# Kernel optimization log

Hardware: AMD Instinct MI355X
Metric: run time of the kernel (lower is better)

Reference implementation:

```python
import jax, jax.numpy as jnp
import numpy as np

H, W = 85, 85
N_HEAD = 8

def layernorm(x, g, b, eps=1e-5):
    m = x.mean(-1, keepdims=True)
    v = ((x - m) ** 2).mean(-1, keepdims=True)
    return (x - m) * jax.lax.rsqrt(v + eps) * g + b


def setup_inputs() -> dict:
    key = jax.random.key(0)
    ks = jax.random.split(key, 12)
    B, C = 8, 256
    N = H * W
    hd = C // N_HEAD
    Ch = C * 4  # mlp_ratio = 4
    init = lambda k, fan_in, sh: (jax.random.normal(k, sh, jnp.float32) / np.float32(np.sqrt(fan_in)))
    d = {}
    d['fx'] = jax.random.normal(ks[0], (B, N, C), jnp.float32)
    # ln_1
    d['ln1_g'] = jnp.ones((C,), jnp.float32); d['ln1_b'] = jnp.zeros((C,), jnp.float32)
    # Galerkin linear attention projections (per-head split of C)
    d['Wq'] = init(ks[1], C, (C, C)); d['bq'] = jnp.zeros((C,), jnp.float32)
    d['Wk'] = init(ks[2], C, (C, C)); d['bk'] = jnp.zeros((C,), jnp.float32)
    d['Wv'] = init(ks[3], C, (C, C)); d['bv'] = jnp.zeros((C,), jnp.float32)
    d['Wo'] = init(ks[4], C, (C, C)); d['bo'] = jnp.zeros((C,), jnp.float32)
    # per-head LayerNorms on K and V (Galerkin normalization replacing softmax)
    d['kln_g'] = jnp.ones((N_HEAD, hd), jnp.float32); d['kln_b'] = jnp.zeros((N_HEAD, hd), jnp.float32)
    d['vln_g'] = jnp.ones((N_HEAD, hd), jnp.float32); d['vln_b'] = jnp.zeros((N_HEAD, hd), jnp.float32)
    # ln_2
    d['ln2_g'] = jnp.ones((C,), jnp.float32); d['ln2_b'] = jnp.zeros((C,), jnp.float32)
    # MLP (n_layers=0, res=False): pre linear + gelu, post linear
    d['W1'] = init(ks[5], C, (C, Ch)); d['b1'] = jnp.zeros((Ch,), jnp.float32)
    d['W2'] = init(ks[6], Ch, (Ch, C)); d['b2'] = jnp.zeros((C,), jnp.float32)
    return d


def reference(fx, ln1_g, ln1_b, Wq, bq, Wk, bk, Wv, bv, Wo, bo,
              kln_g, kln_b, vln_g, vln_b, ln2_g, ln2_b, W1, b1, W2, b2):
    B, N, C = fx.shape
    hd = C // N_HEAD
    x = layernorm(fx, ln1_g, ln1_b)  # [B,N,C]
    # (permute/reshape to image grid and back is a no-op for per-token attention math)
    split = lambda t: t.reshape(B, N, N_HEAD, hd).transpose(0, 2, 1, 3)  # [B,h,N,d]
    q = split(x @ Wq + bq)
    k = split(x @ Wk + bk)
    v = split(x @ Wv + bv)
    # Galerkin: LayerNorm on K and V over head dim, no softmax
    k = layernorm(k, kln_g[None, :, None, :], kln_b[None, :, None, :])
    v = layernorm(v, vln_g[None, :, None, :], vln_b[None, :, None, :])
    kv = jnp.einsum('bhnd,bhne->bhde', k, v) / N  # [B,h,d,d]
    attn = jnp.einsum('bhnd,bhde->bhne', q, kv)   # [B,h,N,d]
    attn = attn.transpose(0, 2, 1, 3).reshape(B, N, C)
    attn = attn @ Wo + bo
    fx = fx + attn  # residual 1
    x2 = layernorm(fx, ln2_g, ln2_b)
    x2 = jax.nn.gelu(x2 @ W1 + b1) @ W2 + b2
    return fx + x2  # residual 2
```

## Files before the change

### kernel.cpp

```cpp
#include <hip/hip_runtime.h>
#include <hip/hip_bf16.h>
#include <stdint.h>

#define B_ 8
#define NTOK 7225
#define MTOT (B_*NTOK)
#define MROWS 58368
#define RT_FULL 452
#define RT_BATCH 57

typedef unsigned short u16;
typedef u16 u16x8 __attribute__((ext_vector_type(8)));
typedef u16 u16x4 __attribute__((ext_vector_type(4)));
typedef __bf16 bf16x8 __attribute__((ext_vector_type(8)));
typedef float f32x4 __attribute__((ext_vector_type(4)));

__device__ inline float bf2f(u16 u){ union{float f;uint32_t i;}c; c.i=((uint32_t)u)<<16; return c.f; }
__device__ inline u16 f2bf(float f){ union{float f;uint32_t i;}c; c.f=f; uint32_t x=c.i;
                                     return (u16)((x + 0x7fffu + ((x>>16)&1u))>>16); }
__device__ inline uint32_t cvt_pk_bf16(float a, float b){
  uint32_t r; asm("v_cvt_pk_bf16_f32 %0, %1, %2" : "=v"(r) : "v"(a), "v"(b)); return r;
}
__device__ inline float gelu_f(float x){
  float t = 0.7978845608028654f * x * (1.0f + 0.044715f*x*x);
  float e = __expf(2.0f*t);
  return x * (1.0f - __builtin_amdgcn_rcpf(e + 1.0f));
}

__device__ inline void gload_lds16(const u16* g, u16* l) {
  __builtin_amdgcn_global_load_lds(
      (__attribute__((address_space(1))) void*)(const_cast<u16*>(g)),
      (__attribute__((address_space(3))) void*)(l), 16, 0, 0);
}

template<int EPI>
__global__ __launch_bounds__(256)
void gemm_bt(const u16* __restrict__ A, int lda,
             const u16* __restrict__ B, int ldb, int bStride,
             const float* __restrict__ bias,
             const float* __restrict__ res,
             void* __restrict__ outp, int ldo,
             int K, int rowsValid, int batchRowStride)
{
  __shared__ alignas(16) u16 As[2][128][32];
  __shared__ alignas(16) u16 Bs[2][128][32];
  const int tid = threadIdx.x;
  const int wid = tid >> 6;
  const int lane = tid & 63;

  const int gx = gridDim.x, gy = gridDim.y;
  const int n = gx * gy;
  const int flat = blockIdx.y * gx + blockIdx.x;
  const int qq = n >> 3, rr = n & 7;
  const int xcd = flat & 7, pos = flat >> 3;
  const int swz = (xcd < rr ? xcd*(qq+1) : rr*(qq+1) + (xcd-rr)*qq) + pos;
  const int bx = swz / gy, by = swz % gy;

  const int bz = blockIdx.z;
  const long rowBase = (long)bz * batchRowStride + (long)bx * 128;
  const int colBase = by * 128;
  const u16* Bp = B + (long)bz * bStride;

  const int srow = lane >> 2;
  const int scol = ((lane & 3) ^ ((lane >> 3) & 3)) * 8;
  const int NTk = K >> 5;

  auto stage = [&](int bf, int kt) {
    const int k0 = kt << 5;
#pragma unroll
    for (int i = 0; i < 2; ++i) {
      int r = wid*32 + i*16 + srow;
      gload_lds16(A + (rowBase + r)*(long)lda + k0 + scol, &As[bf][wid*32 + i*16][0]);
    }
#pragma unroll
    for (int i = 0; i < 2; ++i) {
      int r = wid*32 + i*16 + srow;
      gload_lds16(Bp + (long)(colBase + r)*ldb + k0 + scol, &Bs[bf][wid*32 + i*16][0]);
    }
  };

  f32x4 acc[4][4] = {};
  const int wm = wid >> 1, wn = wid & 1;
  const int lr = lane & 15;
  const int sl = lane >> 4;

  stage(0, 0);
  for (int kt = 0; kt < NTk; ++kt) {
    const int bf = kt & 1;
    __syncthreads();
    if (kt + 1 < NTk) stage(bf ^ 1, kt + 1);
    bf16x8 a[4], b[4];
#pragma unroll
    for (int mi = 0; mi < 4; ++mi) {
      const int r = wm*64 + mi*16 + lr;
      const int sp = sl ^ ((r >> 1) & 3);
      a[mi] = *reinterpret_cast<const bf16x8*>(&As[bf][r][sp*8]);
    }
#pragma unroll
    for (int ni = 0; ni < 4; ++ni) {
      const int r = wn*64 + ni*16 + lr;
      const int sp = sl ^ ((r >> 1) & 3);
      b[ni] = *reinterpret_cast<const bf16x8*>(&Bs[bf][r][sp*8]);
    }
#pragma unroll
    for (int mi = 0; mi < 4; ++mi)
#pragma unroll
      for (int ni = 0; ni < 4; ++ni)
        acc[mi][ni] = __builtin_amdgcn_mfma_f32_16x16x32_bf16(b[ni], a[mi], acc[mi][ni], 0, 0, 0);
  }

  const int cq = (lane >> 4) * 4;
  f32x4 bv4[4];
#pragma unroll
  for (int ni = 0; ni < 4; ++ni)
    bv4[ni] = *reinterpret_cast<const f32x4*>(&bias[colBase + wn*64 + ni*16 + cq]);
#pragma unroll
  for (int mi = 0; mi < 4; ++mi) {
    const int r = wm*64 + mi*16 + lr;
    if (bx*128 + r < rowsValid) {
      const long grow = rowBase + r;
#pragma unroll
      for (int ni = 0; ni < 4; ++ni) {
        const int c0 = colBase + wn*64 + ni*16 + cq;
        const long oidx = grow*(long)ldo + c0;
        f32x4 v = acc[mi][ni] + bv4[ni];
        if (EPI == 0) {
          uint2 pk; pk.x = cvt_pk_bf16(v[0], v[1]); pk.y = cvt_pk_bf16(v[2], v[3]);
          *reinterpret_cast<uint2*>((u16*)outp + oidx) = pk;
        } else if (EPI == 1) {
          uint2 pk; pk.x = cvt_pk_bf16(gelu_f(v[0]), gelu_f(v[1]));
          pk.y = cvt_pk_bf16(gelu_f(v[2]), gelu_f(v[3]));
          *reinterpret_cast<uint2*>((u16*)outp + oidx) = pk;
        } else {
          f32x4 rv = *reinterpret_cast<const f32x4*>((const float*)res + oidx);
          *reinterpret_cast<f32x4*>((float*)outp + oidx) = v + rv;
        }
      }
    }
  }
}

__global__ __launch_bounds__(256)
void ln_kernel(const float* __restrict__ in, const float* __restrict__ g,
               const float* __restrict__ bt, u16* __restrict__ out, int M)
{
  const int wv = threadIdx.x >> 6, lane = threadIdx.x & 63;
  const int t = blockIdx.x * 4 + wv;
  if (t >= M) return;
  const float4 x = reinterpret_cast<const float4*>(in + (long)t*256)[lane];
  float s = x.x + x.y + x.z + x.w;
  float q = x.x*x.x + x.y*x.y + x.z*x.z + x.w*x.w;
#pragma unroll
  for (int o = 32; o > 0; o >>= 1) { s += __shfl_xor(s, o); q += __shfl_xor(q, o); }
  const float m  = s * (1.0f/256.0f);
  const float var = q * (1.0f/256.0f) - m*m;
  const float rs = rsqrtf(var + 1e-5f);
  const float4 gv = reinterpret_cast<const float4*>(g)[lane];
  const float4 bv = reinterpret_cast<const float4*>(bt)[lane];
  uint2 o4;
  o4.x = cvt_pk_bf16((x.x - m)*rs*gv.x + bv.x, (x.y - m)*rs*gv.y + bv.y);
  o4.y = cvt_pk_bf16((x.z - m)*rs*gv.z + bv.z, (x.w - m)*rs*gv.w + bv.w);
  *reinterpret_cast<uint2*>(out + (long)t*256 + lane*4) = o4;
}

__global__ __launch_bounds__(256)
void kv_kernel(const u16* __restrict__ QKV,
               const float* __restrict__ kg, const float* __restrict__ kb,
               const float* __restrict__ vg, const float* __restrict__ vb,
               float* __restrict__ kvout)
{
  const int bh = blockIdx.x, b = bh >> 3, h = bh & 7;
  const int tid = threadIdx.x;
  __shared__ u16 kls[256][32];
  __shared__ u16 vls[256][32];
  __shared__ float sg[4][32];
  if (tid < 32) {
    sg[0][tid] = kg[h*32 + tid];
    sg[1][tid] = kb[h*32 + tid];
    sg[2][tid] = vg[h*32 + tid];
    sg[3][tid] = vb[h*32 + tid];
  }
  const int d = tid >> 3, e0 = (tid & 7) * 4;
  float a0=0, a1=0, a2=0, a3=0;

  for (int sub = 0; sub < 2; ++sub) {
    const int r = blockIdx.y * 512 + sub * 256 + tid;
    __syncthreads();
    if (r < NTOK) {
      const u16* rowp = QKV + (long)(b*NTOK + r)*768;
#pragma unroll
      for (int kv2 = 0; kv2 < 2; ++kv2) {
        const u16* p = rowp + (kv2 ? 512 : 256) + h*32;
        float xv[32]; float s = 0.f;
#pragma unroll
        for (int q4 = 0; q4 < 4; ++q4) {
          u16x8 u = *reinterpret_cast<const u16x8*>(p + q4*8);
#pragma unroll
          for (int j = 0; j < 8; ++j) { float f = bf2f(u[j]); xv[q4*8+j] = f; s += f; }
        }
        const float m = s * (1.0f/32.0f);
        float vv = 0.f;
#pragma unroll
        for (int j = 0; j < 32; ++j) { float d2 = xv[j]-m; vv += d2*d2; }
        const float rs = rsqrtf(vv*(1.0f/32.0f) + 1e-5f);
        const float* gg = sg[kv2 ? 2 : 0];
        const float* bb = sg[kv2 ? 3 : 1];
        u16 (*dst)[32] = kv2 ? vls : kls;
#pragma unroll
        for (int j = 0; j < 32; ++j) dst[tid][j] = f2bf((xv[j]-m)*rs*gg[j] + bb[j]);
      }
    } else {
#pragma unroll
      for (int j = 0; j < 32; ++j) { kls[tid][j] = 0; vls[tid][j] = 0; }
    }
    __syncthreads();
#pragma unroll 4
    for (int rr = 0; rr < 256; ++rr) {
      const float kd = bf2f(kls[rr][d]);
      u16x4 v4 = *reinterpret_cast<const u16x4*>(&vls[rr][e0]);
      a0 += kd * bf2f(v4[0]); a1 += kd * bf2f(v4[1]);
      a2 += kd * bf2f(v4[2]); a3 += kd * bf2f(v4[3]);
    }
  }
  const float sc = 1.0f / (float)NTOK;
  float* o = kvout + (long)bh*1024 + d*32 + e0;
  atomicAdd(o+0, a0*sc); atomicAdd(o+1, a1*sc);
  atomicAdd(o+2, a2*sc); atomicAdd(o+3, a3*sc);
}

__global__ __launch_bounds__(256)
void woeff_kernel(const float* __restrict__ kv, const float* __restrict__ Wo,
                  u16* __restrict__ Woet)
{
  const int b = blockIdx.x >> 8, c = blockIdx.x & 255;
  const int rtid = threadIdx.x;
  const int h = rtid >> 5, dd = rtid & 31;
  const float* kvp = kv + ((long)(b*8 + h)*32 + dd)*32;
  float s = 0.f;
#pragma unroll 8
  for (int e = 0; e < 32; ++e) s += kvp[e] * Wo[(h*32 + e)*256 + c];
  Woet[(long)(b*256 + c)*256 + rtid] = f2bf(s);
}

__global__ void zero_f32(float* p, int n) {
  int i = blockIdx.x*blockDim.x + threadIdx.x; if (i < n) p[i] = 0.f;
}
__global__ void concat_bias(const float* bq, const float* bk, const float* bv, float* o) {
  int i = threadIdx.x;
  o[i] = (i < 256) ? bq[i] : ((i < 512) ? bk[i-256] : bv[i-512]);
}
__global__ __launch_bounds__(256)
void transpose_cvt(const float* __restrict__ src, u16* __restrict__ dst, int R, int C) {
  __shared__ float t[32][33];
  const int tc = blockIdx.x * 32, tr = blockIdx.y * 32;
  const int lx = threadIdx.x & 31, ly = threadIdx.x >> 5;
#pragma unroll
  for (int i = 0; i < 32; i += 8)
    t[ly + i][lx] = src[(long)(tr + ly + i)*C + tc + lx];
  __syncthreads();
#pragma unroll
  for (int i = 0; i < 32; i += 8)
    dst[(long)(tc + ly + i)*R + tr + lx] = f2bf(t[lx][ly + i]);
}

extern "C" void kernel_launch(void* const* d_in, const int* in_sizes, int n_in,
                              void* d_out, int out_size, void* d_ws, size_t ws_size,
                              hipStream_t stream)
{
  const float* fx    = (const float*)d_in[0];
  const float* ln1_g = (const float*)d_in[1];
  const float* ln1_b = (const float*)d_in[2];
  const float* Wq = (const float*)d_in[3];
  const float* bq = (const float*)d_in[4];
  const float* Wk = (const float*)d_in[5];
  const float* bk = (const float*)d_in[6];
  const float* Wv = (const float*)d_in[7];
  const float* bv = (const float*)d_in[8];
  const float* Wo = (const float*)d_in[9];
  const float* bo = (const float*)d_in[10];
  const float* kg  = (const float*)d_in[11];
  const float* kbb = (const float*)d_in[12];
  const float* vg  = (const float*)d_in[13];
  const float* vbb = (const float*)d_in[14];
  const float* ln2_g = (const float*)d_in[15];
  const float* ln2_b = (const float*)d_in[16];
  const float* W1 = (const float*)d_in[17];
  const float* b1 = (const float*)d_in[18];
  const float* W2 = (const float*)d_in[19];
  const float* b2 = (const float*)d_in[20];
  float* outF = (float*)d_out;

  char* ws = (char*)d_ws;
  size_t off = 0;
  auto alloc = [&](size_t bytes) { char* p = ws + off; off += (bytes + 255) & ~(size_t)255; return p; };
  u16* bufX   = (u16*)alloc((size_t)MROWS*256*2);
  u16* bufQKV = (u16*)alloc((size_t)MROWS*768*2);
  u16* bufH   = (u16*)alloc((size_t)MROWS*1024*2);
  u16* Wqkv_t = (u16*)alloc(768*256*2);
  u16* W1_t   = (u16*)alloc(1024*256*2);
  u16* W2_t   = (u16*)alloc(256*1024*2);
  u16* Woe_t  = (u16*)alloc((size_t)8*256*256*2);
  float* kvb  = (float*)alloc((size_t)64*1024*4);
  float* bqkv = (float*)alloc(768*4);
  (void)ws_size; (void)out_size; (void)n_in; (void)in_sizes;

  zero_f32<<<256, 256, 0, stream>>>(kvb, 65536);
  concat_bias<<<1, 768, 0, stream>>>(bq, bk, bv, bqkv);
  transpose_cvt<<<dim3(8,8),  256, 0, stream>>>(Wq, Wqkv_t,          256, 256);
  transpose_cvt<<<dim3(8,8),  256, 0, stream>>>(Wk, Wqkv_t + 65536,  256, 256);
  transpose_cvt<<<dim3(8,8),  256, 0, stream>>>(Wv, Wqkv_t + 131072, 256, 256);
  transpose_cvt<<<dim3(32,8), 256, 0, stream>>>(W1, W1_t, 256, 1024);
  transpose_cvt<<<dim3(8,32), 256, 0, stream>>>(W2, W2_t, 1024, 256);

  ln_kernel<<<MTOT/4, 256, 0, stream>>>(fx, ln1_g, ln1_b, bufX, MTOT);

  gemm_bt<0><<<dim3(RT_FULL, 6, 1), 256, 0, stream>>>(
      bufX, 256, Wqkv_t, 256, 0, bqkv, nullptr, bufQKV, 768, 256, 1<<30, 0);

  kv_kernel<<<dim3(64, 15), 256, 0, stream>>>(bufQKV, kg, kbb, vg, vbb, kvb);

  woeff_kernel<<<2048, 256, 0, stream>>>(kvb, Wo, Woe_t);

  gemm_bt<2><<<dim3(RT_BATCH, 2, 8), 256, 0, stream>>>(
      bufQKV, 768, Woe_t, 256, 65536, bo, fx, outF, 256, 256, NTOK, NTOK);

  ln_kernel<<<MTOT/4, 256, 0, stream>>>(outF, ln2_g, ln2_b, bufX, MTOT);

  gemm_bt<1><<<dim3(RT_FULL, 8, 1), 256, 0, stream>>>(
      bufX, 256, W1_t, 256, 0, b1, nullptr, bufH, 1024, 256, 1<<30, 0);

  gemm_bt<2><<<dim3(RT_FULL, 2, 1), 256, 0, stream>>>(
      bufH, 1024, W2_t, 1024, 0, b2, outF, outF, 256, 1024, MTOT, 0);
}
```

Measured before the change: 331.4 us.

## Deepen GEMM LDS pipeline to four buffers with explicit vmcnt waits

The bf16 GEMM's LDS staging goes from double buffering to a four-slot ring that keeps three K-tiles of global-to-LDS loads in flight. The per-iteration __syncthreads is replaced by explicit s_waitcnt vmcnt counts, a raw barrier and a sched_barrier, with the last two tiles handled in a peeled epilogue. The aim is to hide global memory latency behind MFMA work. In exchange, shared memory per block doubles to 64 KB, which can lower occupancy, and correctness now depends on the hand-counted vmcnt values matching the four loads each stage issues.

```diff
diff --git a/kernel.cpp b/kernel.cpp
--- a/kernel.cpp
+++ b/kernel.cpp
@@ -42,8 +42,8 @@
              void* __restrict__ outp, int ldo,
              int K, int rowsValid, int batchRowStride)
 {
-  __shared__ alignas(16) u16 As[2][128][32];
-  __shared__ alignas(16) u16 Bs[2][128][32];
+  __shared__ alignas(16) u16 As[4][128][32];
+  __shared__ alignas(16) u16 Bs[4][128][32];
   const int tid = threadIdx.x;
   const int wid = tid >> 6;
   const int lane = tid & 63;
@@ -65,17 +65,17 @@
   const int scol = ((lane & 3) ^ ((lane >> 3) & 3)) * 8;
   const int NTk = K >> 5;
 
-  auto stage = [&](int bf, int kt) {
+  auto stage = [&](int bi, int kt) {
     const int k0 = kt << 5;
 #pragma unroll
     for (int i = 0; i < 2; ++i) {
       int r = wid*32 + i*16 + srow;
-      gload_lds16(A + (rowBase + r)*(long)lda + k0 + scol, &As[bf][wid*32 + i*16][0]);
+      gload_lds16(A + (rowBase + r)*(long)lda + k0 + scol, &As[bi][wid*32 + i*16][0]);
     }
 #pragma unroll
     for (int i = 0; i < 2; ++i) {
       int r = wid*32 + i*16 + srow;
-      gload_lds16(Bp + (long)(colBase + r)*ldb + k0 + scol, &Bs[bf][wid*32 + i*16][0]);
+      gload_lds16(Bp + (long)(colBase + r)*ldb + k0 + scol, &Bs[bi][wid*32 + i*16][0]);
     }
   };
 
@@ -84,30 +84,44 @@
   const int lr = lane & 15;
   const int sl = lane >> 4;
 
-  stage(0, 0);
-  for (int kt = 0; kt < NTk; ++kt) {
-    const int bf = kt & 1;
-    __syncthreads();
-    if (kt + 1 < NTk) stage(bf ^ 1, kt + 1);
+  auto compute = [&](int bi) {
     bf16x8 a[4], b[4];
 #pragma unroll
     for (int mi = 0; mi < 4; ++mi) {
       const int r = wm*64 + mi*16 + lr;
       const int sp = sl ^ ((r >> 1) & 3);
-      a[mi] = *reinterpret_cast<const bf16x8*>(&As[bf][r][sp*8]);
+      a[mi] = *reinterpret_cast<const bf16x8*>(&As[bi][r][sp*8]);
     }
 #pragma unroll
     for (int ni = 0; ni < 4; ++ni) {
       const int r = wn*64 + ni*16 + lr;
       const int sp = sl ^ ((r >> 1) & 3);
-      b[ni] = *reinterpret_cast<const bf16x8*>(&Bs[bf][r][sp*8]);
+      b[ni] = *reinterpret_cast<const bf16x8*>(&Bs[bi][r][sp*8]);
     }
 #pragma unroll
     for (int mi = 0; mi < 4; ++mi)
 #pragma unroll
       for (int ni = 0; ni < 4; ++ni)
         acc[mi][ni] = __builtin_amdgcn_mfma_f32_16x16x32_bf16(b[ni], a[mi], acc[mi][ni], 0, 0, 0);
+  };
+
+  stage(0, 0); stage(1, 1); stage(2, 2);
+
+  for (int kt = 0; kt < NTk - 2; ++kt) {
+    asm volatile("s_waitcnt vmcnt(8)" ::: "memory");
+    __builtin_amdgcn_s_barrier();
+    __builtin_amdgcn_sched_barrier(0);
+    if (kt < NTk - 3) stage((kt + 3) & 3, kt + 3);
+    compute(kt & 3);
   }
+  asm volatile("s_waitcnt vmcnt(4)" ::: "memory");
+  __builtin_amdgcn_s_barrier();
+  __builtin_amdgcn_sched_barrier(0);
+  compute((NTk - 2) & 3);
+  asm volatile("s_waitcnt vmcnt(0)" ::: "memory");
+  __builtin_amdgcn_s_barrier();
+  __builtin_amdgcn_sched_barrier(0);
+  compute((NTk - 1) & 3);
 
   const int cq = (lane >> 4) * 4;
   f32x4 bv4[4];
```

New measurement: 340.9 us. 1.03x slower.

## Replace tiled GEMMs with persistent streaming GEMM using 128-wide K chunks

Applied to the files above, without the earlier changes.

Swaps the per-tile 256-thread GEMM grid for a persistent kernel of 256 blocks × 512 threads. Each block walks a contiguous range of output tiles as one continuous stream of 128-wide K chunks, double-buffered in 128 KB of LDS with direct global-to-LDS loads and explicit vmcnt waits. The aim is to overlap the loads for the next tile with the math and epilogue of the current one, and to cut launch and tail overhead. In exchange, LDS use rises sharply, occupancy drops to one block per CU, and each wave holds fewer accumulators (32×64), so it has to hide latency mainly through prefetch depth.

```diff
diff --git a/kernel.cpp b/kernel.cpp
--- a/kernel.cpp
+++ b/kernel.cpp
@@ -6,8 +6,6 @@
 #define NTOK 7225
 #define MTOT (B_*NTOK)
 #define MROWS 58368
-#define RT_FULL 452
-#define RT_BATCH 57
 
 typedef unsigned short u16;
 typedef u16 u16x8 __attribute__((ext_vector_type(8)));
@@ -33,107 +31,133 @@
       (__attribute__((address_space(3))) void*)(l), 16, 0, 0);
 }
 
-template<int EPI>
-__global__ __launch_bounds__(256)
-void gemm_bt(const u16* __restrict__ A, int lda,
-             const u16* __restrict__ B, int ldb, int bStride,
-             const float* __restrict__ bias,
-             const float* __restrict__ res,
-             void* __restrict__ outp, int ldo,
-             int K, int rowsValid, int batchRowStride)
-{
-  __shared__ alignas(16) u16 As[2][128][32];
-  __shared__ alignas(16) u16 Bs[2][128][32];
+template<int EPI, int NC>
+__global__ __launch_bounds__(512)
+void gemm_stream(const u16* __restrict__ A, int lda,
+                 const u16* __restrict__ Bm, int ldb, long bStride,
+                 const float* __restrict__ bias,
+                 const float* __restrict__ res,
+                 void* __restrict__ outp, int ldo,
+                 int ntM, int ntN, int nTiles,
+                 int rowsValid, int batchRowStride)
+{
+  __shared__ alignas(16) u16 lds[2][32768];
   const int tid = threadIdx.x;
-  const int wid = tid >> 6;
-  const int lane = tid & 63;
-
-  const int gx = gridDim.x, gy = gridDim.y;
-  const int n = gx * gy;
-  const int flat = blockIdx.y * gx + blockIdx.x;
-  const int qq = n >> 3, rr = n & 7;
-  const int xcd = flat & 7, pos = flat >> 3;
-  const int swz = (xcd < rr ? xcd*(qq+1) : rr*(qq+1) + (xcd-rr)*qq) + pos;
-  const int bx = swz / gy, by = swz % gy;
-
-  const int bz = blockIdx.z;
-  const long rowBase = (long)bz * batchRowStride + (long)bx * 128;
-  const int colBase = by * 128;
-  const u16* Bp = B + (long)bz * bStride;
-
-  const int srow = lane >> 2;
-  const int scol = ((lane & 3) ^ ((lane >> 3) & 3)) * 8;
-  const int NTk = K >> 5;
-
-  auto stage = [&](int bf, int kt) {
-    const int k0 = kt << 5;
-#pragma unroll
-    for (int i = 0; i < 2; ++i) {
-      int r = wid*32 + i*16 + srow;
-      gload_lds16(A + (rowBase + r)*(long)lda + k0 + scol, &As[bf][wid*32 + i*16][0]);
-    }
-#pragma unroll
-    for (int i = 0; i < 2; ++i) {
-      int r = wid*32 + i*16 + srow;
-      gload_lds16(Bp + (long)(colBase + r)*ldb + k0 + scol, &Bs[bf][wid*32 + i*16][0]);
+  const int wid = tid >> 6, lane = tid & 63;
+  const int wm = wid >> 1, wn = wid & 1;
+  const int lr = lane & 15, sl = lane >> 4;
+
+  const int nb = gridDim.x;
+  const int q = nTiles / nb, rem = nTiles % nb;
+  const int p = blockIdx.x;
+  const int t0 = p * q + (p < rem ? p : rem);
+  const int myT = q + (p < rem ? 1 : 0);
+  const int U = myT * NC;
+
+  auto stage = [&](int u, int bi) {
+    const int t = t0 + u / NC, ch = u % NC;
+    int rel = t; const int bz = rel / (ntM*ntN); rel -= bz*(ntM*ntN);
+    const int bx = rel / ntN, by = rel - bx*ntN;
+    const long rowB = (long)bz * batchRowStride + (long)bx * 128;
+    const long colB = (long)by * 128;
+    const u16* Bp = Bm + (long)bz * bStride;
+    const int k0 = ch << 7;
+#pragma unroll
+    for (int i = 0; i < 4; ++i) {
+      const int o16 = i*512 + tid;
+      const int r = o16 >> 4, ps = o16 & 15;
+      const int gc = ((ps ^ (r & 7)) << 3) + k0;
+      gload_lds16(A + (rowB + r)*(long)lda + gc, &lds[bi][o16*8]);
+    }
+#pragma unroll
+    for (int i = 0; i < 4; ++i) {
+      const int o16 = i*512 + tid;
+      const int r = o16 >> 4, ps = o16 & 15;
+      const int gc = ((ps ^ (r & 7)) << 3) + k0;
+      gload_lds16(Bp + (colB + r)*(long)ldb + gc, &lds[bi][16384 + o16*8]);
     }
   };
 
-  f32x4 acc[4][4] = {};
-  const int wm = wid >> 1, wn = wid & 1;
-  const int lr = lane & 15;
-  const int sl = lane >> 4;
-
+  f32x4 acc[2][4];
   stage(0, 0);
-  for (int kt = 0; kt < NTk; ++kt) {
-    const int bf = kt & 1;
-    __syncthreads();
-    if (kt + 1 < NTk) stage(bf ^ 1, kt + 1);
-    bf16x8 a[4], b[4];
-#pragma unroll
-    for (int mi = 0; mi < 4; ++mi) {
-      const int r = wm*64 + mi*16 + lr;
-      const int sp = sl ^ ((r >> 1) & 3);
-      a[mi] = *reinterpret_cast<const bf16x8*>(&As[bf][r][sp*8]);
+  stage(1, 1);
+
+  for (int u = 0; u < U; ++u) {
+    const int bi = u & 1;
+    const int ch = u % NC;
+    if (u == U - 1) { asm volatile("s_waitcnt vmcnt(0)" ::: "memory"); }
+    else            { asm volatile("s_waitcnt vmcnt(8)" ::: "memory"); }
+    __builtin_amdgcn_s_barrier();
+
+    if (ch == 0) {
+#pragma unroll
+      for (int mi = 0; mi < 2; ++mi)
+#pragma unroll
+        for (int ni = 0; ni < 4; ++ni) acc[mi][ni] = f32x4{0.f,0.f,0.f,0.f};
+    }
+
+    bf16x8 fa[2][4], fb[4][4];
+#pragma unroll
+    for (int mi = 0; mi < 2; ++mi) {
+      const int ra = wm*32 + mi*16 + lr;
+#pragma unroll
+      for (int ks = 0; ks < 4; ++ks) {
+        const int ps = (ks*4 + sl) ^ (ra & 7);
+        fa[mi][ks] = *reinterpret_cast<const bf16x8*>(&lds[bi][ra*128 + ps*8]);
+      }
     }
 #pragma unroll
     for (int ni = 0; ni < 4; ++ni) {
-      const int r = wn*64 + ni*16 + lr;
-      const int sp = sl ^ ((r >> 1) & 3);
-      b[ni] = *reinterpret_cast<const bf16x8*>(&Bs[bf][r][sp*8]);
-    }
-#pragma unroll
-    for (int mi = 0; mi < 4; ++mi)
-#pragma unroll
-      for (int ni = 0; ni < 4; ++ni)
-        acc[mi][ni] = __builtin_amdgcn_mfma_f32_16x16x32_bf16(b[ni], a[mi], acc[mi][ni], 0, 0, 0);
-  }
-
-  const int cq = (lane >> 4) * 4;
-  f32x4 bv4[4];
-#pragma unroll
-  for (int ni = 0; ni < 4; ++ni)
-    bv4[ni] = *reinterpret_cast<const f32x4*>(&bias[colBase + wn*64 + ni*16 + cq]);
-#pragma unroll
-  for (int mi = 0; mi < 4; ++mi) {
-    const int r = wm*64 + mi*16 + lr;
-    if (bx*128 + r < rowsValid) {
-      const long grow = rowBase + r;
-#pragma unroll
-      for (int ni = 0; ni < 4; ++ni) {
-        const int c0 = colBase + wn*64 + ni*16 + cq;
-        const long oidx = grow*(long)ldo + c0;
-        f32x4 v = acc[mi][ni] + bv4[ni];
-        if (EPI == 0) {
-          uint2 pk; pk.x = cvt_pk_bf16(v[0], v[1]); pk.y = cvt_pk_bf16(v[2], v[3]);
-          *reinterpret_cast<uint2*>((u16*)outp + oidx) = pk;
-        } else if (EPI == 1) {
-          uint2 pk; pk.x = cvt_pk_bf16(gelu_f(v[0]), gelu_f(v[1]));
-          pk.y = cvt_pk_bf16(gelu_f(v[2]), gelu_f(v[3]));
-          *reinterpret_cast<uint2*>((u16*)outp + oidx) = pk;
-        } else {
-          f32x4 rv = *reinterpret_cast<const f32x4*>((const float*)res + oidx);
-          *reinterpret_cast<f32x4*>((float*)outp + oidx) = v + rv;
+      const int rb = wn*64 + ni*16 + lr;
+#pragma unroll
+      for (int ks = 0; ks < 4; ++ks) {
+        const int ps = (ks*4 + sl) ^ (rb & 7);
+        fb[ni][ks] = *reinterpret_cast<const bf16x8*>(&lds[bi][16384 + rb*128 + ps*8]);
+      }
+    }
+    asm volatile("s_waitcnt lgkmcnt(0)" ::: "memory");
+    __builtin_amdgcn_sched_barrier(0);
+    __builtin_amdgcn_s_barrier();
+
+    if (u + 2 < U) stage(u + 2, bi);
+
+#pragma unroll
+    for (int ks = 0; ks < 4; ++ks)
+#pragma unroll
+      for (int mi = 0; mi < 2; ++mi)
+#pragma unroll
+        for (int ni = 0; ni < 4; ++ni)
+          acc[mi][ni] = __builtin_amdgcn_mfma_f32_16x16x32_bf16(fb[ni][ks], fa[mi][ks], acc[mi][ni], 0, 0, 0);
+
+    if (ch == NC - 1) {
+      const int t = t0 + u / NC;
+      int rel = t; const int bz = rel / (ntM*ntN); rel -= bz*(ntM*ntN);
+      const int bx = rel / ntN, by = rel - bx*ntN;
+      const long rowB = (long)bz * batchRowStride + (long)bx * 128;
+      const int colB = by * 128;
+      const int cq = sl * 4;
+#pragma unroll
+      for (int mi = 0; mi < 2; ++mi) {
+        const int r = wm*32 + mi*16 + lr;
+        if (bx*128 + r < rowsValid) {
+          const long grow = rowB + r;
+#pragma unroll
+          for (int ni = 0; ni < 4; ++ni) {
+            const int c0 = colB + wn*64 + ni*16 + cq;
+            const long oidx = grow*(long)ldo + c0;
+            f32x4 v = acc[mi][ni] + *reinterpret_cast<const f32x4*>(&bias[c0]);
+            if (EPI == 0) {
+              uint2 pk; pk.x = cvt_pk_bf16(v[0], v[1]); pk.y = cvt_pk_bf16(v[2], v[3]);
+              *reinterpret_cast<uint2*>((u16*)outp + oidx) = pk;
+            } else if (EPI == 1) {
+              uint2 pk; pk.x = cvt_pk_bf16(gelu_f(v[0]), gelu_f(v[1]));
+              pk.y = cvt_pk_bf16(gelu_f(v[2]), gelu_f(v[3]));
+              *reinterpret_cast<uint2*>((u16*)outp + oidx) = pk;
+            } else {
+              f32x4 rv = *reinterpret_cast<const f32x4*>((const float*)res + oidx);
+              *reinterpret_cast<f32x4*>((float*)outp + oidx) = v + rv;
+            }
+          }
         }
       }
     }
@@ -314,21 +338,25 @@
 
   ln_kernel<<<MTOT/4, 256, 0, stream>>>(fx, ln1_g, ln1_b, bufX, MTOT);
 
-  gemm_bt<0><<<dim3(RT_FULL, 6, 1), 256, 0, stream>>>(
-      bufX, 256, Wqkv_t, 256, 0, bqkv, nullptr, bufQKV, 768, 256, 1<<30, 0);
+  gemm_stream<0,2><<<256, 512, 0, stream>>>(
+      bufX, 256, Wqkv_t, 256, 0, bqkv, nullptr, bufQKV, 768,
+      452, 6, 452*6, MTOT, 0);
 
   kv_kernel<<<dim3(64, 15), 256, 0, stream>>>(bufQKV, kg, kbb, vg, vbb, kvb);
 
   woeff_kernel<<<2048, 256, 0, stream>>>(kvb, Wo, Woe_t);
 
-  gemm_bt<2><<<dim3(RT_BATCH, 2, 8), 256, 0, stream>>>(
-      bufQKV, 768, Woe_t, 256, 65536, bo, fx, outF, 256, 256, NTOK, NTOK);
+  gemm_stream<2,2><<<256, 512, 0, stream>>>(
+      bufQKV, 768, Woe_t, 256, 65536, bo, fx, outF, 256,
+      57, 2, 8*57*2, NTOK, NTOK);
 
   ln_kernel<<<MTOT/4, 256, 0, stream>>>(outF, ln2_g, ln2_b, bufX, MTOT);
 
-  gemm_bt<1><<<dim3(RT_FULL, 8, 1), 256, 0, stream>>>(
-      bufX, 256, W1_t, 256, 0, b1, nullptr, bufH, 1024, 256, 1<<30, 0);
-
-  gemm_bt<2><<<dim3(RT_FULL, 2, 1), 256, 0, stream>>>(
-      bufH, 1024, W2_t, 1024, 0, b2, outF, outF, 256, 1024, MTOT, 0);
-}
+  gemm_stream<1,2><<<256, 512, 0, stream>>>(
+      bufX, 256, W1_t, 256, 0, b1, nullptr, bufH, 1024,
+      452, 8, 452*8, MTOT, 0);
+
+  gemm_stream<2,8><<<256, 512, 0, stream>>>(
+      bufH, 1024, W2_t, 1024, 0, b2, outF, outF, 256,
+      452, 2, 452*2, MTOT, 0);
+}
```

New measurement: 391.1 us. 1.18x slower.

## Fold Q projection into per-batch attention weight and enlarge GEMM tiles

Applied to the files above, without the earlier changes.

Removes the Q projection GEMM by precomputing, per batch, a combined matrix Watt = Wq·(kv·Wo) and a bias be = bq·(kv·Wo) + bo. The attention output GEMM then reads the LN1 output directly instead of stored Q, and the QKV GEMM shrinks to a KV-only GEMM. Separately, the GEMM kernel moves to 256x256 tiles with 512 threads and a K-step of 64 to raise data reuse per block. The larger tiles use more registers and shared memory and leave fewer blocks in flight, and the combined weight is rounded to bf16, which adds rounding error.

```diff
diff --git a/kernel.cpp b/kernel.cpp
--- a/kernel.cpp
+++ b/kernel.cpp
@@ -6,8 +6,8 @@
 #define NTOK 7225
 #define MTOT (B_*NTOK)
 #define MROWS 58368
-#define RT_FULL 452
-#define RT_BATCH 57
+#define MT_FULL 226
+#define MT_BATCH 29
 
 typedef unsigned short u16;
 typedef u16 u16x8 __attribute__((ext_vector_type(8)));
@@ -34,19 +34,19 @@
 }
 
 template<int EPI>
-__global__ __launch_bounds__(256)
-void gemm_bt(const u16* __restrict__ A, int lda,
-             const u16* __restrict__ B, int ldb, int bStride,
-             const float* __restrict__ bias,
+__global__ __launch_bounds__(512, 2)
+void gemm256(const u16* __restrict__ A, int lda,
+             const u16* __restrict__ Bm, int ldb, long bStride,
+             const float* __restrict__ bias, int biasStride,
              const float* __restrict__ res,
              void* __restrict__ outp, int ldo,
              int K, int rowsValid, int batchRowStride)
 {
-  __shared__ alignas(16) u16 As[2][128][32];
-  __shared__ alignas(16) u16 Bs[2][128][32];
+  __shared__ alignas(16) u16 As[2][2][256][32];
+  __shared__ alignas(16) u16 Bs[2][2][256][32];
   const int tid = threadIdx.x;
-  const int wid = tid >> 6;
-  const int lane = tid & 63;
+  const int wid = tid >> 6, lane = tid & 63;
+  const int wm = wid >> 2, wn = wid & 3;
 
   const int gx = gridDim.x, gy = gridDim.y;
   const int n = gx * gy;
@@ -55,75 +55,76 @@
   const int xcd = flat & 7, pos = flat >> 3;
   const int swz = (xcd < rr ? xcd*(qq+1) : rr*(qq+1) + (xcd-rr)*qq) + pos;
   const int bx = swz / gy, by = swz % gy;
-
   const int bz = blockIdx.z;
-  const long rowBase = (long)bz * batchRowStride + (long)bx * 128;
-  const int colBase = by * 128;
-  const u16* Bp = B + (long)bz * bStride;
+
+  const long rowBase = (long)bz * batchRowStride + (long)bx * 256;
+  const int colBase = by * 256;
+  const u16* Bp = Bm + (long)bz * bStride;
+  const float* biasP = bias + bz * biasStride;
 
   const int srow = lane >> 2;
   const int scol = ((lane & 3) ^ ((lane >> 3) & 3)) * 8;
-  const int NTk = K >> 5;
+  const int NT = K >> 6;
 
   auto stage = [&](int bf, int kt) {
-    const int k0 = kt << 5;
-#pragma unroll
-    for (int i = 0; i < 2; ++i) {
-      int r = wid*32 + i*16 + srow;
-      gload_lds16(A + (rowBase + r)*(long)lda + k0 + scol, &As[bf][wid*32 + i*16][0]);
-    }
-#pragma unroll
-    for (int i = 0; i < 2; ++i) {
-      int r = wid*32 + i*16 + srow;
-      gload_lds16(Bp + (long)(colBase + r)*ldb + k0 + scol, &Bs[bf][wid*32 + i*16][0]);
+    const int k0 = kt << 6;
+#pragma unroll
+    for (int i = 0; i < 4; ++i) {
+      const int u = wid*4 + i;
+      const int sub = u >> 4, r0 = (u & 15) * 16;
+      const int r = r0 + srow;
+      gload_lds16(A + (rowBase + r)*(long)lda + k0 + sub*32 + scol, &As[bf][sub][r0][0]);
+    }
+#pragma unroll
+    for (int i = 0; i < 4; ++i) {
+      const int u = wid*4 + i;
+      const int sub = u >> 4, r0 = (u & 15) * 16;
+      const int r = r0 + srow;
+      gload_lds16(Bp + (long)(colBase + r)*ldb + k0 + sub*32 + scol, &Bs[bf][sub][r0][0]);
     }
   };
 
-  f32x4 acc[4][4] = {};
-  const int wm = wid >> 1, wn = wid & 1;
+  f32x4 acc[8][4] = {};
   const int lr = lane & 15;
   const int sl = lane >> 4;
+  const int sp = (sl ^ ((lr >> 1) & 3)) * 8;
+
+  auto compute = [&](int bf) {
+#pragma unroll
+    for (int sub = 0; sub < 2; ++sub) {
+      bf16x8 a[8], b[4];
+#pragma unroll
+      for (int mi = 0; mi < 8; ++mi)
+        a[mi] = *reinterpret_cast<const bf16x8*>(&As[bf][sub][wm*128 + mi*16 + lr][sp]);
+#pragma unroll
+      for (int ni = 0; ni < 4; ++ni)
+        b[ni] = *reinterpret_cast<const bf16x8*>(&Bs[bf][sub][wn*64 + ni*16 + lr][sp]);
+#pragma unroll
+      for (int mi = 0; mi < 8; ++mi)
+#pragma unroll
+        for (int ni = 0; ni < 4; ++ni)
+          acc[mi][ni] = __builtin_amdgcn_mfma_f32_16x16x32_bf16(b[ni], a[mi], acc[mi][ni], 0, 0, 0);
+    }
+  };
 
   stage(0, 0);
-  for (int kt = 0; kt < NTk; ++kt) {
-    const int bf = kt & 1;
+  for (int kt = 0; kt < NT; ++kt) {
     __syncthreads();
-    if (kt + 1 < NTk) stage(bf ^ 1, kt + 1);
-    bf16x8 a[4], b[4];
-#pragma unroll
-    for (int mi = 0; mi < 4; ++mi) {
-      const int r = wm*64 + mi*16 + lr;
-      const int sp = sl ^ ((r >> 1) & 3);
-      a[mi] = *reinterpret_cast<const bf16x8*>(&As[bf][r][sp*8]);
-    }
-#pragma unroll
-    for (int ni = 0; ni < 4; ++ni) {
-      const int r = wn*64 + ni*16 + lr;
-      const int sp = sl ^ ((r >> 1) & 3);
-      b[ni] = *reinterpret_cast<const bf16x8*>(&Bs[bf][r][sp*8]);
-    }
-#pragma unroll
-    for (int mi = 0; mi < 4; ++mi)
-#pragma unroll
-      for (int ni = 0; ni < 4; ++ni)
-        acc[mi][ni] = __builtin_amdgcn_mfma_f32_16x16x32_bf16(b[ni], a[mi], acc[mi][ni], 0, 0, 0);
-  }
-
-  const int cq = (lane >> 4) * 4;
-  f32x4 bv4[4];
-#pragma unroll
-  for (int ni = 0; ni < 4; ++ni)
-    bv4[ni] = *reinterpret_cast<const f32x4*>(&bias[colBase + wn*64 + ni*16 + cq]);
-#pragma unroll
-  for (int mi = 0; mi < 4; ++mi) {
-    const int r = wm*64 + mi*16 + lr;
-    if (bx*128 + r < rowsValid) {
+    if (kt + 1 < NT) stage((kt + 1) & 1, kt + 1);
+    compute(kt & 1);
+  }
+
+  const int cq = sl * 4;
+#pragma unroll
+  for (int mi = 0; mi < 8; ++mi) {
+    const int r = wm*128 + mi*16 + lr;
+    if (bx*256 + r < rowsValid) {
       const long grow = rowBase + r;
 #pragma unroll
       for (int ni = 0; ni < 4; ++ni) {
         const int c0 = colBase + wn*64 + ni*16 + cq;
         const long oidx = grow*(long)ldo + c0;
-        f32x4 v = acc[mi][ni] + bv4[ni];
+        f32x4 v = acc[mi][ni] + *reinterpret_cast<const f32x4*>(&biasP[c0]);
         if (EPI == 0) {
           uint2 pk; pk.x = cvt_pk_bf16(v[0], v[1]); pk.y = cvt_pk_bf16(v[2], v[3]);
           *reinterpret_cast<uint2*>((u16*)outp + oidx) = pk;
@@ -164,7 +165,7 @@
 }
 
 __global__ __launch_bounds__(256)
-void kv_kernel(const u16* __restrict__ QKV,
+void kv_kernel(const u16* __restrict__ KV,
                const float* __restrict__ kg, const float* __restrict__ kb,
                const float* __restrict__ vg, const float* __restrict__ vb,
                float* __restrict__ kvout)
@@ -187,10 +188,10 @@
     const int r = blockIdx.y * 512 + sub * 256 + tid;
     __syncthreads();
     if (r < NTOK) {
-      const u16* rowp = QKV + (long)(b*NTOK + r)*768;
+      const u16* rowp = KV + (long)(b*NTOK + r)*512;
 #pragma unroll
       for (int kv2 = 0; kv2 < 2; ++kv2) {
-        const u16* p = rowp + (kv2 ? 512 : 256) + h*32;
+        const u16* p = rowp + (kv2 ? 256 : 0) + h*32;
         float xv[32]; float s = 0.f;
 #pragma unroll
         for (int q4 = 0; q4 < 4; ++q4) {
@@ -242,12 +243,50 @@
   Woet[(long)(b*256 + c)*256 + rtid] = f2bf(s);
 }
 
+__global__ __launch_bounds__(256)
+void watt_kernel(const u16* __restrict__ wq_bf, const u16* __restrict__ Woet,
+                 u16* __restrict__ Watt)
+{
+  const int b = blockIdx.x >> 8, c = blockIdx.x & 255;
+  const int k = threadIdx.x;
+  const u16* wr = wq_bf + (long)k*256;
+  const u16* er = Woet + ((long)(b*256 + c))*256;
+  float s = 0.f;
+#pragma unroll 4
+  for (int j0 = 0; j0 < 256; j0 += 8) {
+    u16x8 wv = *reinterpret_cast<const u16x8*>(wr + j0);
+    u16x8 ev = *reinterpret_cast<const u16x8*>(er + j0);
+#pragma unroll
+    for (int j = 0; j < 8; ++j) s += bf2f(wv[j]) * bf2f(ev[j]);
+  }
+  Watt[((long)(b*256 + c))*256 + k] = f2bf(s);
+}
+
+__global__ __launch_bounds__(256)
+void be_kernel(const float* __restrict__ bq, const float* __restrict__ bo,
+               const u16* __restrict__ Woet, float* __restrict__ be)
+{
+  const int b = blockIdx.x, c = threadIdx.x;
+  const u16* er = Woet + ((long)(b*256 + c))*256;
+  float s = bo[c];
+#pragma unroll 4
+  for (int j0 = 0; j0 < 256; j0 += 8) {
+    u16x8 ev = *reinterpret_cast<const u16x8*>(er + j0);
+#pragma unroll
+    for (int j = 0; j < 8; ++j) s += bq[j0+j] * bf2f(ev[j]);
+  }
+  be[b*256 + c] = s;
+}
+
 __global__ void zero_f32(float* p, int n) {
   int i = blockIdx.x*blockDim.x + threadIdx.x; if (i < n) p[i] = 0.f;
 }
-__global__ void concat_bias(const float* bq, const float* bk, const float* bv, float* o) {
+__global__ void concat_bias2(const float* bk, const float* bv, float* o) {
   int i = threadIdx.x;
-  o[i] = (i < 256) ? bq[i] : ((i < 512) ? bk[i-256] : bv[i-512]);
+  o[i] = (i < 256) ? bk[i] : bv[i-256];
+}
+__global__ void cvt_bf(const float* __restrict__ src, u16* __restrict__ dst, int n) {
+  int i = blockIdx.x*blockDim.x + threadIdx.x; if (i < n) dst[i] = f2bf(src[i]);
 }
 __global__ __launch_bounds__(256)
 void transpose_cvt(const float* __restrict__ src, u16* __restrict__ dst, int R, int C) {
@@ -294,41 +333,46 @@
   size_t off = 0;
   auto alloc = [&](size_t bytes) { char* p = ws + off; off += (bytes + 255) & ~(size_t)255; return p; };
   u16* bufX   = (u16*)alloc((size_t)MROWS*256*2);
-  u16* bufQKV = (u16*)alloc((size_t)MROWS*768*2);
+  u16* bufKV  = (u16*)alloc((size_t)MROWS*512*2);
   u16* bufH   = (u16*)alloc((size_t)MROWS*1024*2);
-  u16* Wqkv_t = (u16*)alloc(768*256*2);
+  u16* Wkv_t  = (u16*)alloc(512*256*2);
   u16* W1_t   = (u16*)alloc(1024*256*2);
   u16* W2_t   = (u16*)alloc(256*1024*2);
   u16* Woe_t  = (u16*)alloc((size_t)8*256*256*2);
+  u16* Watt   = (u16*)alloc((size_t)8*256*256*2);
+  u16* wq_bf  = (u16*)alloc(256*256*2);
   float* kvb  = (float*)alloc((size_t)64*1024*4);
-  float* bqkv = (float*)alloc(768*4);
+  float* bkv  = (float*)alloc(512*4);
+  float* be   = (float*)alloc(8*256*4);
   (void)ws_size; (void)out_size; (void)n_in; (void)in_sizes;
 
   zero_f32<<<256, 256, 0, stream>>>(kvb, 65536);
-  concat_bias<<<1, 768, 0, stream>>>(bq, bk, bv, bqkv);
-  transpose_cvt<<<dim3(8,8),  256, 0, stream>>>(Wq, Wqkv_t,          256, 256);
-  transpose_cvt<<<dim3(8,8),  256, 0, stream>>>(Wk, Wqkv_t + 65536,  256, 256);
-  transpose_cvt<<<dim3(8,8),  256, 0, stream>>>(Wv, Wqkv_t + 131072, 256, 256);
+  concat_bias2<<<1, 512, 0, stream>>>(bk, bv, bkv);
+  cvt_bf<<<256, 256, 0, stream>>>(Wq, wq_bf, 65536);
+  transpose_cvt<<<dim3(8,8),  256, 0, stream>>>(Wk, Wkv_t,         256, 256);
+  transpose_cvt<<<dim3(8,8),  256, 0, stream>>>(Wv, Wkv_t + 65536, 256, 256);
   transpose_cvt<<<dim3(32,8), 256, 0, stream>>>(W1, W1_t, 256, 1024);
   transpose_cvt<<<dim3(8,32), 256, 0, stream>>>(W2, W2_t, 1024, 256);
 
   ln_kernel<<<MTOT/4, 256, 0, stream>>>(fx, ln1_g, ln1_b, bufX, MTOT);
 
-  gemm_bt<0><<<dim3(RT_FULL, 6, 1), 256, 0, stream>>>(
-      bufX, 256, Wqkv_t, 256, 0, bqkv, nullptr, bufQKV, 768, 256, 1<<30, 0);
-
-  kv_kernel<<<dim3(64, 15), 256, 0, stream>>>(bufQKV, kg, kbb, vg, vbb, kvb);
+  gemm256<0><<<dim3(MT_FULL, 2, 1), 512, 0, stream>>>(
+      bufX, 256, Wkv_t, 256, 0, bkv, 0, nullptr, bufKV, 512, 256, MTOT, 0);
+
+  kv_kernel<<<dim3(64, 15), 256, 0, stream>>>(bufKV, kg, kbb, vg, vbb, kvb);
 
   woeff_kernel<<<2048, 256, 0, stream>>>(kvb, Wo, Woe_t);
-
-  gemm_bt<2><<<dim3(RT_BATCH, 2, 8), 256, 0, stream>>>(
-      bufQKV, 768, Woe_t, 256, 65536, bo, fx, outF, 256, 256, NTOK, NTOK);
+  watt_kernel<<<2048, 256, 0, stream>>>(wq_bf, Woe_t, Watt);
+  be_kernel<<<8, 256, 0, stream>>>(bq, bo, Woe_t, be);
+
+  gemm256<2><<<dim3(MT_BATCH, 1, 8), 512, 0, stream>>>(
+      bufX, 256, Watt, 256, 65536, be, 256, fx, outF, 256, 256, NTOK, NTOK);
 
   ln_kernel<<<MTOT/4, 256, 0, stream>>>(outF, ln2_g, ln2_b, bufX, MTOT);
 
-  gemm_bt<1><<<dim3(RT_FULL, 8, 1), 256, 0, stream>>>(
-      bufX, 256, W1_t, 256, 0, b1, nullptr, bufH, 1024, 256, 1<<30, 0);
-
-  gemm_bt<2><<<dim3(RT_FULL, 2, 1), 256, 0, stream>>>(
-      bufH, 1024, W2_t, 1024, 0, b2, outF, outF, 256, 1024, MTOT, 0);
-}
+  gemm256<1><<<dim3(MT_FULL, 4, 1), 512, 0, stream>>>(
+      bufX, 256, W1_t, 256, 0, b1, 0, nullptr, bufH, 1024, 256, MTOT, 0);
+
+  gemm256<2><<<dim3(MT_FULL, 1, 1), 512, 0, stream>>>(
+      bufH, 1024, W2_t, 1024, 0, b2, 0, outF, outF, 256, 1024, MTOT, 0);
+}
```

Result: slower. 374.7 us (+13.1%).
